# Optimization experiments

Measured on AMD Instinct MI355X. Metric: run time of the kernel, lower is better.

Reference implementation:

```python
import jax, jax.numpy as jnp
import numpy as np
import math

B, S, HID, NH = 4, 2048, 1024, 16
HD = HID // NH  # head dim = 64


def setup_inputs() -> dict:
    key = jax.random.key(0)
    ks = jax.random.split(key, 8)
    sc = 0.02
    return {
        "x": jax.random.normal(ks[0], (B, S, HID), dtype=jnp.float32),
        "att_mask": jnp.zeros((B, 1, 1, S), dtype=jnp.float32),
        "Wq": jax.random.normal(ks[1], (HID, HID), dtype=jnp.float32) * sc,
        "bq": jax.random.normal(ks[2], (HID,), dtype=jnp.float32) * sc,
        "Wk": jax.random.normal(ks[3], (HID, HID), dtype=jnp.float32) * sc,
        "bk": jax.random.normal(ks[4], (HID,), dtype=jnp.float32) * sc,
        "Wv": jax.random.normal(ks[5], (HID, HID), dtype=jnp.float32) * sc,
        "bv": jax.random.normal(ks[6], (HID,), dtype=jnp.float32) * sc,
    }


def reference(x, att_mask, Wq, bq, Wk, bk, Wv, bv):
    # quant_mode=False path: QuantLinear acts as a plain affine projection
    # (the running min/max stats only calibrate `scale`, which is unused in
    # the float path), and IntSoftmax reduces to a standard softmax.
    q = x @ Wq.T + bq  # [B,S,HID]
    k = x @ Wk.T + bk
    v = x @ Wv.T + bv
    # split heads: [B,S,HID] -> [B,NH,S,HD]
    q = q.reshape(B, S, NH, HD).transpose(0, 2, 1, 3)
    k = k.reshape(B, S, NH, HD).transpose(0, 2, 1, 3)
    v = v.reshape(B, S, NH, HD).transpose(0, 2, 1, 3)
    scores = jnp.einsum("bhqd,bhkd->bhqk", q, k) / math.sqrt(HD) + att_mask
    probs = jax.nn.softmax(scores, axis=-1)  # [B,NH,S,S]
    ctx = jnp.einsum("bhqk,bhkd->bhqd", probs, v)  # [B,NH,S,HD]
    return ctx.transpose(0, 2, 1, 3).reshape(B, S, HID)
```

## Files before the change

kernel.cpp:

```cpp
#include <hip/hip_runtime.h>
#include <hip/hip_bf16.h>
#include <cstdint>
#include <cstddef>

#define BB   4
#define SS   2048
#define HIDD 1024
#define NHH  16
#define HDD  64
#define MM   (BB*SS)
#define L2E  1.4426950408889634f
#define SH4  5.770780163555854f

typedef __bf16    bf16x8 __attribute__((ext_vector_type(8)));
typedef float     f32x4  __attribute__((ext_vector_type(4)));
typedef _Float16  half4  __attribute__((ext_vector_type(4)));
typedef _Float16  half2v __attribute__((ext_vector_type(2)));

__device__ __forceinline__ unsigned short f2b(float f) {
    unsigned u = __builtin_bit_cast(unsigned, f);
    return (unsigned short)((u + 0x7FFFu + ((u >> 16) & 1u)) >> 16);
}

__device__ __forceinline__ half2v pkrtz(float a, float b) {
    return __builtin_bit_cast(half2v, __builtin_amdgcn_cvt_pkrtz(a, b));
}

__device__ __forceinline__ void gl_lds16(const void* g, void* l) {
    __builtin_amdgcn_global_load_lds(
        (const __attribute__((address_space(1))) void*)g,
        (__attribute__((address_space(3))) void*)l, 16, 0, 0);
}

#define NX4 (MM * HIDD / 4)
#define NW4 (HIDD * HIDD / 4)
__global__ __launch_bounds__(256) void cvt_all(
    const float* __restrict__ x,  const float* __restrict__ wq,
    const float* __restrict__ wk, const float* __restrict__ wv,
    unsigned short* __restrict__ xb, unsigned short* __restrict__ wb)
{
    int i = blockIdx.x * 256 + threadIdx.x;
    const float* src; unsigned short* dst; int off;
    if (i < NX4) { src = x; dst = xb; off = i; }
    else {
        int j = i - NX4;
        int w = j >> 18;
        off = j & (NW4 - 1);
        src = (w == 0) ? wq : (w == 1) ? wk : wv;
        dst = wb + (size_t)w * HIDD * HIDD;
    }
    float4 v = reinterpret_cast<const float4*>(src)[off];
    ushort4 o;
    o.x = f2b(v.x); o.y = f2b(v.y); o.z = f2b(v.z); o.w = f2b(v.w);
    reinterpret_cast<ushort4*>(dst)[off] = o;
}

__global__ __launch_bounds__(256, 3) void qkv_gemm(
    const unsigned short* __restrict__ xb,
    const unsigned short* __restrict__ wb,
    const float* __restrict__ bq, const float* __restrict__ bk, const float* __restrict__ bv,
    unsigned short* __restrict__ Qb, unsigned short* __restrict__ Kb,
    _Float16* __restrict__ Vtb)
{
    __shared__ unsigned short lA[128 * 64];
    __shared__ unsigned short lB[128 * 64];

    const int tid  = threadIdx.x;
    const int wave = tid >> 6, lane = tid & 63;
    const int lh   = lane & 15, quad = lane >> 4;
    const int l7   = lh & 7;
    const int m0   = blockIdx.x * 128;
    const int opn  = blockIdx.y;
    const int op   = opn >> 3;
    const int n0   = (opn & 7) * 128;
    const unsigned short* W = wb + (size_t)op * HIDD * HIDD;
    const float* bias = (op == 0) ? bq : (op == 1) ? bk : bv;

    f32x4 acc[4][4];
#pragma unroll
    for (int i = 0; i < 4; i++)
#pragma unroll
        for (int j = 0; j < 4; j++) acc[i][j] = f32x4{0.f, 0.f, 0.f, 0.f};

    const int wm = wave & 1, wn = wave >> 1;
    const unsigned short* srcA = (op == 2) ? lA : lB;
    const unsigned short* srcB = (op == 2) ? lB : lA;
    const int offA = (op == 2) ? wm : wn;
    const int offB = (op == 2) ? wn : wm;

    const int srow = tid >> 3;
    const int sg   = tid & 7;

    for (int k0 = 0; k0 < HIDD; k0 += 64) {
#pragma unroll
        for (int rr = 0; rr < 4; rr++) {
            const int row = srow + rr * 32;
            const int gcol = k0 + ((sg ^ (row & 7)) << 3);
            gl_lds16(&xb[(size_t)(m0 + row) * HIDD + gcol], &lA[row * 64 + sg * 8]);
            gl_lds16(&W [(size_t)(n0 + row) * HIDD + gcol], &lB[row * 64 + sg * 8]);
        }
        __syncthreads();

#pragma unroll
        for (int kk = 0; kk < 2; kk++) {
            bf16x8 aF[4], bF[4];
#pragma unroll
            for (int i = 0; i < 4; i++) {
                const int row = offA * 64 + i * 16 + lh;
                aF[i] = *reinterpret_cast<const bf16x8*>(
                    &srcA[row * 64 + (((kk * 4 + quad) ^ l7) << 3)]);
            }
#pragma unroll
            for (int j = 0; j < 4; j++) {
                const int row = offB * 64 + j * 16 + lh;
                bF[j] = *reinterpret_cast<const bf16x8*>(
                    &srcB[row * 64 + (((kk * 4 + quad) ^ l7) << 3)]);
            }
#pragma unroll
            for (int i = 0; i < 4; i++)
#pragma unroll
                for (int j = 0; j < 4; j++)
                    acc[i][j] = __builtin_amdgcn_mfma_f32_16x16x32_bf16(aF[i], bF[j], acc[i][j], 0, 0, 0);
        }
        __syncthreads();
    }

    if (op == 2) {
#pragma unroll
        for (int j = 0; j < 4; j++) {
            const int n = n0 + offB * 64 + j * 16 + lh;
            const float bvv = bias[n];
            const int h = n >> 6, d = n & 63;
#pragma unroll
            for (int i = 0; i < 4; i++) {
                const int mrow = m0 + offA * 64 + i * 16 + quad * 4;
                const int b_ = mrow >> 11, s_ = mrow & 2047;
                half2v h01 = pkrtz(acc[i][j][0] + bvv, acc[i][j][1] + bvv);
                half2v h23 = pkrtz(acc[i][j][2] + bvv, acc[i][j][3] + bvv);
                half4 hv; hv[0] = h01[0]; hv[1] = h01[1]; hv[2] = h23[0]; hv[3] = h23[1];
                size_t a = ((size_t)(b_ * NHH + h) * HDD + d) * SS + s_;
                *reinterpret_cast<half4*>(&Vtb[a]) = hv;
            }
        }
    } else {
        const float qs = (op == 0) ? (0.125f * L2E) : 1.0f;
        unsigned short* dst = (op == 0) ? Qb : Kb;
#pragma unroll
        for (int i = 0; i < 4; i++) {
            const int nb = n0 + offA * 64 + i * 16 + quad * 4;
            const float4 bb = *reinterpret_cast<const float4*>(&bias[nb]);
            const int h = nb >> 6, d = nb & 63;
#pragma unroll
            for (int j = 0; j < 4; j++) {
                const int m = m0 + offB * 64 + j * 16 + lh;
                const int b_ = m >> 11, s_ = m & 2047;
                ushort4 o;
                o.x = f2b((acc[i][j][0] + bb.x) * qs);
                o.y = f2b((acc[i][j][1] + bb.y) * qs);
                o.z = f2b((acc[i][j][2] + bb.z) * qs);
                o.w = f2b((acc[i][j][3] + bb.w) * qs);
                *reinterpret_cast<ushort4*>(
                    &dst[((size_t)(b_ * NHH + h) * SS + s_) * HDD + d]) = o;
            }
        }
    }
}

__global__ __launch_bounds__(256, 4) void attn_kernel(
    const unsigned short* __restrict__ Qb,
    const unsigned short* __restrict__ Kb,
    const _Float16* __restrict__ Vtb,
    const float* __restrict__ mask,
    float* __restrict__ out)
{
    __shared__ unsigned short lK[2][64 * 64];
    __shared__ _Float16      lV[2][64 * 64];

    const int tid  = threadIdx.x;
    const int wave = tid >> 6, lane = tid & 63;
    const int lh   = lane & 15, quad = lane >> 4;
    const int l7   = lh & 7;
    const int bh = blockIdx.x, qt = blockIdx.y;
    const int b = bh >> 4, h = bh & 15;
    const unsigned short* Qh = Qb  + (size_t)bh * SS * HDD;
    const unsigned short* Kh = Kb  + (size_t)bh * SS * HDD;
    const _Float16*       Vh = Vtb + (size_t)bh * HDD * SS;
    const float* mk = mask + (size_t)b * SS;
    const int q0 = qt * 128;

    bf16x8 qF[2][2];
#pragma unroll
    for (int i = 0; i < 2; i++)
#pragma unroll
        for (int kk = 0; kk < 2; kk++)
            qF[i][kk] = *reinterpret_cast<const bf16x8*>(
                &Qh[(size_t)(q0 + wave * 32 + i * 16 + lh) * HDD + kk * 32 + quad * 8]);

    f32x4 oacc[2][4];
#pragma unroll
    for (int i = 0; i < 2; i++)
#pragma unroll
        for (int dj = 0; dj < 4; dj++) oacc[i][dj] = f32x4{0.f, 0.f, 0.f, 0.f};
    float ls[2] = {0.f, 0.f};

    const int srow = tid >> 3;
    const int sg   = tid & 7;

#define STAGE(KT, BUF) do {                                                     \
    const int kb_ = (KT) * 64;                                                  \
    _Pragma("unroll")                                                           \
    for (int rr = 0; rr < 2; rr++) {                                            \
        const int row = srow + rr * 32;                                         \
        const int sw = ((sg ^ (row & 7)) << 3);                                 \
        gl_lds16(&Kh[(size_t)(kb_ + row) * HDD + sw], &lK[BUF][row * 64 + sg * 8]); \
        gl_lds16(&Vh[(size_t)row * SS + kb_ + sw],    &lV[BUF][row * 64 + sg * 8]); \
    }                                                                           \
} while (0)

    STAGE(0, 0);
    __syncthreads();

    for (int kt = 0; kt < SS / 64; kt++) {
        if (kt < SS / 64 - 1) STAGE(kt + 1, (kt + 1) & 1);
        const int buf = kt & 1;
        const int kb = kt * 64;

        float4 mg[4];
#pragma unroll
        for (int c = 0; c < 4; c++)
            mg[c] = *reinterpret_cast<const float4*>(&mk[kb + c * 16 + quad * 4]);

        half4 pf[4][2];
#pragma unroll
        for (int c = 0; c < 4; c++) {
            const int krow = (c * 16 + lh) * 64;
            bf16x8 kf0 = *reinterpret_cast<const bf16x8*>(&lK[buf][krow + ((quad ^ l7) << 3)]);
            bf16x8 kf1 = *reinterpret_cast<const bf16x8*>(&lK[buf][krow + (((4 + quad) ^ l7) << 3)]);
            f32x4 mm;
            mm[0] = __builtin_fmaf(mg[c].x, L2E, -SH4);
            mm[1] = __builtin_fmaf(mg[c].y, L2E, -SH4);
            mm[2] = __builtin_fmaf(mg[c].z, L2E, -SH4);
            mm[3] = __builtin_fmaf(mg[c].w, L2E, -SH4);
#pragma unroll
            for (int i = 0; i < 2; i++) {
                f32x4 s = __builtin_amdgcn_mfma_f32_16x16x32_bf16(kf0, qF[i][0], mm, 0, 0, 0);
                s = __builtin_amdgcn_mfma_f32_16x16x32_bf16(kf1, qF[i][1], s, 0, 0, 0);
                float e0 = __builtin_amdgcn_exp2f(s[0]);
                float e1 = __builtin_amdgcn_exp2f(s[1]);
                float e2 = __builtin_amdgcn_exp2f(s[2]);
                float e3 = __builtin_amdgcn_exp2f(s[3]);
                ls[i] += (e0 + e1) + (e2 + e3);
                half2v p01 = pkrtz(e0, e1);
                half2v p23 = pkrtz(e2, e3);
                half4 p; p[0] = p01[0]; p[1] = p01[1]; p[2] = p23[0]; p[3] = p23[1];
                pf[c][i] = p;
            }
        }

#pragma unroll
        for (int c = 0; c < 4; c++) {
            const int vg = (c * 2 + (quad >> 1)) ^ l7;
            half4 vf[4];
#pragma unroll
            for (int dj = 0; dj < 4; dj++)
                vf[dj] = *reinterpret_cast<const half4*>(
                    &lV[buf][(dj * 16 + lh) * 64 + (vg << 3) + (quad & 1) * 4]);
#pragma unroll
            for (int i = 0; i < 2; i++)
#pragma unroll
                for (int dj = 0; dj < 4; dj++)
                    oacc[i][dj] = __builtin_amdgcn_mfma_f32_16x16x16f16(vf[dj], pf[c][i], oacc[i][dj], 0, 0, 0);
        }
        if (kt < SS / 64 - 1) __syncthreads();
    }

    float rls[2];
#pragma unroll
    for (int i = 0; i < 2; i++) {
        float l = ls[i];
        l += __shfl_xor(l, 16);
        l += __shfl_xor(l, 32);
        rls[i] = 1.0f / l;
    }
#pragma unroll
    for (int i = 0; i < 2; i++) {
        const int q = q0 + wave * 32 + i * 16 + lh;
#pragma unroll
        for (int dj = 0; dj < 4; dj++) {
            float4 o4;
            o4.x = oacc[i][dj][0] * rls[i];
            o4.y = oacc[i][dj][1] * rls[i];
            o4.z = oacc[i][dj][2] * rls[i];
            o4.w = oacc[i][dj][3] * rls[i];
            *reinterpret_cast<float4*>(
                &out[((size_t)b * SS + q) * HIDD + h * HDD + dj * 16 + quad * 4]) = o4;
        }
    }
}

extern "C" void kernel_launch(void* const* d_in, const int* in_sizes, int n_in,
                              void* d_out, int out_size, void* d_ws, size_t ws_size,
                              hipStream_t stream) {
    const float* x    = (const float*)d_in[0];
    const float* mask = (const float*)d_in[1];
    const float* Wq   = (const float*)d_in[2];
    const float* bq   = (const float*)d_in[3];
    const float* Wk   = (const float*)d_in[4];
    const float* bk   = (const float*)d_in[5];
    const float* Wv   = (const float*)d_in[6];
    const float* bv   = (const float*)d_in[7];
    float* out = (float*)d_out;
    (void)in_sizes; (void)n_in; (void)out_size; (void)ws_size;

    unsigned short* ws  = (unsigned short*)d_ws;
    unsigned short* xb  = ws;
    unsigned short* wb  = xb + (size_t)MM * HIDD;
    unsigned short* Qb  = wb + (size_t)3 * HIDD * HIDD;
    unsigned short* Kb  = Qb + (size_t)MM * HIDD;
    _Float16*       Vtb = (_Float16*)(Kb + (size_t)MM * HIDD);

    cvt_all<<<(NX4 + 3 * NW4) / 256, 256, 0, stream>>>(x, Wq, Wk, Wv, xb, wb);

    qkv_gemm<<<dim3(MM / 128, 24), 256, 0, stream>>>(xb, wb, bq, bk, bv, Qb, Kb, Vtb);

    attn_kernel<<<dim3(BB * NHH, SS / 128), 256, 0, stream>>>(Qb, Kb, Vtb, mask, out);
}
```

Measured before the change: 242.4 us.

## Software-pipeline QK^T/softmax of next tile with PV of current tile

Restructures the attention loop so the score MFMAs and exp2 for key tile kt+1 are issued in the same iteration as the PV MFMAs for tile kt. Prefetch moves two tiles ahead, and V gets a triple-buffered LDS ring so the V tile still being read is never overwritten. The intent is to overlap the exp/VALU work with the matrix-core work and hide load latency. In exchange it uses more LDS and more registers for the two probability fragment sets, which may reduce occupancy under launch_bounds(256,4).

```diff
diff --git a/kernel.cpp b/kernel.cpp
--- a/kernel.cpp
+++ b/kernel.cpp
@@ -11,6 +11,7 @@
 #define MM   (BB*SS)
 #define L2E  1.4426950408889634f
 #define SH4  5.770780163555854f
+#define NT   (SS / 64)
 
 typedef __bf16    bf16x8 __attribute__((ext_vector_type(8)));
 typedef float     f32x4  __attribute__((ext_vector_type(4)));
@@ -174,7 +175,7 @@
     float* __restrict__ out)
 {
     __shared__ unsigned short lK[2][64 * 64];
-    __shared__ _Float16      lV[2][64 * 64];
+    __shared__ _Float16      lV[3][64 * 64];
 
     const int tid  = threadIdx.x;
     const int wave = tid >> 6, lane = tid & 63;
@@ -206,72 +207,102 @@
     const int srow = tid >> 3;
     const int sg   = tid & 7;
 
-#define STAGE(KT, BUF) do {                                                     \
+#define STAGE_K(KT, BUF) do {                                                   \
     const int kb_ = (KT) * 64;                                                  \
     _Pragma("unroll")                                                           \
     for (int rr = 0; rr < 2; rr++) {                                            \
         const int row = srow + rr * 32;                                         \
         const int sw = ((sg ^ (row & 7)) << 3);                                 \
         gl_lds16(&Kh[(size_t)(kb_ + row) * HDD + sw], &lK[BUF][row * 64 + sg * 8]); \
-        gl_lds16(&Vh[(size_t)row * SS + kb_ + sw],    &lV[BUF][row * 64 + sg * 8]); \
     }                                                                           \
 } while (0)
 
-    STAGE(0, 0);
+#define STAGE_V(KT, SLOT) do {                                                  \
+    const int kb_ = (KT) * 64;                                                  \
+    _Pragma("unroll")                                                           \
+    for (int rr = 0; rr < 2; rr++) {                                            \
+        const int row = srow + rr * 32;                                         \
+        const int sw = ((sg ^ (row & 7)) << 3);                                 \
+        gl_lds16(&Vh[(size_t)row * SS + kb_ + sw], &lV[SLOT][row * 64 + sg * 8]); \
+    }                                                                           \
+} while (0)
+
+#define A_BLOCK(KBN, LKP, PFD) do {                                             \
+    _Pragma("unroll")                                                           \
+    for (int c = 0; c < 4; c++) {                                               \
+        const int krow = (c * 16 + lh) * 64;                                    \
+        bf16x8 kf0 = *reinterpret_cast<const bf16x8*>(&(LKP)[krow + ((quad ^ l7) << 3)]); \
+        bf16x8 kf1 = *reinterpret_cast<const bf16x8*>(&(LKP)[krow + (((4 + quad) ^ l7) << 3)]); \
+        float4 mg = *reinterpret_cast<const float4*>(&mk[(KBN) + c * 16 + quad * 4]); \
+        f32x4 mm;                                                               \
+        mm[0] = __builtin_fmaf(mg.x, L2E, -SH4);                                \
+        mm[1] = __builtin_fmaf(mg.y, L2E, -SH4);                                \
+        mm[2] = __builtin_fmaf(mg.z, L2E, -SH4);                                \
+        mm[3] = __builtin_fmaf(mg.w, L2E, -SH4);                                \
+        _Pragma("unroll")                                                       \
+        for (int i = 0; i < 2; i++) {                                           \
+            f32x4 s = __builtin_amdgcn_mfma_f32_16x16x32_bf16(kf0, qF[i][0], mm, 0, 0, 0); \
+            s = __builtin_amdgcn_mfma_f32_16x16x32_bf16(kf1, qF[i][1], s, 0, 0, 0); \
+            float e0 = __builtin_amdgcn_exp2f(s[0]);                            \
+            float e1 = __builtin_amdgcn_exp2f(s[1]);                            \
+            float e2 = __builtin_amdgcn_exp2f(s[2]);                            \
+            float e3 = __builtin_amdgcn_exp2f(s[3]);                            \
+            ls[i] += (e0 + e1) + (e2 + e3);                                     \
+            half2v p01 = pkrtz(e0, e1);                                         \
+            half2v p23 = pkrtz(e2, e3);                                         \
+            half4 p; p[0] = p01[0]; p[1] = p01[1]; p[2] = p23[0]; p[3] = p23[1]; \
+            (PFD)[c][i] = p;                                                    \
+        }                                                                       \
+    }                                                                           \
+} while (0)
+
+    STAGE_K(0, 0); STAGE_V(0, 0);
+    STAGE_K(1, 1); STAGE_V(1, 1);
     __syncthreads();
 
-    for (int kt = 0; kt < SS / 64; kt++) {
-        if (kt < SS / 64 - 1) STAGE(kt + 1, (kt + 1) & 1);
-        const int buf = kt & 1;
-        const int kb = kt * 64;
-
-        float4 mg[4];
-#pragma unroll
-        for (int c = 0; c < 4; c++)
-            mg[c] = *reinterpret_cast<const float4*>(&mk[kb + c * 16 + quad * 4]);
-
-        half4 pf[4][2];
-#pragma unroll
-        for (int c = 0; c < 4; c++) {
-            const int krow = (c * 16 + lh) * 64;
-            bf16x8 kf0 = *reinterpret_cast<const bf16x8*>(&lK[buf][krow + ((quad ^ l7) << 3)]);
-            bf16x8 kf1 = *reinterpret_cast<const bf16x8*>(&lK[buf][krow + (((4 + quad) ^ l7) << 3)]);
-            f32x4 mm;
-            mm[0] = __builtin_fmaf(mg[c].x, L2E, -SH4);
-            mm[1] = __builtin_fmaf(mg[c].y, L2E, -SH4);
-            mm[2] = __builtin_fmaf(mg[c].z, L2E, -SH4);
-            mm[3] = __builtin_fmaf(mg[c].w, L2E, -SH4);
-#pragma unroll
-            for (int i = 0; i < 2; i++) {
-                f32x4 s = __builtin_amdgcn_mfma_f32_16x16x32_bf16(kf0, qF[i][0], mm, 0, 0, 0);
-                s = __builtin_amdgcn_mfma_f32_16x16x32_bf16(kf1, qF[i][1], s, 0, 0, 0);
-                float e0 = __builtin_amdgcn_exp2f(s[0]);
-                float e1 = __builtin_amdgcn_exp2f(s[1]);
-                float e2 = __builtin_amdgcn_exp2f(s[2]);
-                float e3 = __builtin_amdgcn_exp2f(s[3]);
-                ls[i] += (e0 + e1) + (e2 + e3);
-                half2v p01 = pkrtz(e0, e1);
-                half2v p23 = pkrtz(e2, e3);
-                half4 p; p[0] = p01[0]; p[1] = p01[1]; p[2] = p23[0]; p[3] = p23[1];
-                pf[c][i] = p;
-            }
-        }
-
-#pragma unroll
-        for (int c = 0; c < 4; c++) {
-            const int vg = (c * 2 + (quad >> 1)) ^ l7;
-            half4 vf[4];
-#pragma unroll
-            for (int dj = 0; dj < 4; dj++)
-                vf[dj] = *reinterpret_cast<const half4*>(
-                    &lV[buf][(dj * 16 + lh) * 64 + (vg << 3) + (quad & 1) * 4]);
-#pragma unroll
-            for (int i = 0; i < 2; i++)
+    half4 pf_prev[4][2], pf_cur[4][2];
+    A_BLOCK(0, lK[0], pf_prev);
+    __syncthreads();
+
+    int vs_pv = 0;
+    int vs_st = 2;
+    for (int kt = 0; kt < NT; kt++) {
+        const bool has_next = (kt + 1 < NT);
+        if (kt + 2 < NT) {
+            STAGE_K(kt + 2, kt & 1);
+            STAGE_V(kt + 2, vs_st);
+        }
+        if (has_next) {
+            const unsigned short* lkp = lK[(kt + 1) & 1];
+            A_BLOCK((kt + 1) * 64, lkp, pf_cur);
+        }
+        {
+            const _Float16* lvp = lV[vs_pv];
+#pragma unroll
+            for (int c = 0; c < 4; c++) {
+                const int vg = (c * 2 + (quad >> 1)) ^ l7;
+                half4 vf[4];
 #pragma unroll
                 for (int dj = 0; dj < 4; dj++)
-                    oacc[i][dj] = __builtin_amdgcn_mfma_f32_16x16x16f16(vf[dj], pf[c][i], oacc[i][dj], 0, 0, 0);
-        }
-        if (kt < SS / 64 - 1) __syncthreads();
+                    vf[dj] = *reinterpret_cast<const half4*>(
+                        &lvp[(dj * 16 + lh) * 64 + (vg << 3) + (quad & 1) * 4]);
+#pragma unroll
+                for (int i = 0; i < 2; i++)
+#pragma unroll
+                    for (int dj = 0; dj < 4; dj++)
+                        oacc[i][dj] = __builtin_amdgcn_mfma_f32_16x16x16f16(
+                            vf[dj], pf_prev[c][i], oacc[i][dj], 0, 0, 0);
+            }
+        }
+        if (has_next) {
+            __syncthreads();
+#pragma unroll
+            for (int c = 0; c < 4; c++)
+#pragma unroll
+                for (int i = 0; i < 2; i++) pf_prev[c][i] = pf_cur[c][i];
+        }
+        vs_pv = (vs_pv == 2) ? 0 : vs_pv + 1;
+        vs_st = (vs_st == 2) ? 0 : vs_st + 1;
     }
 
     float rls[2];
```

After: 262.1 us. 8.1% more time.
